# Kernel tuning notes

Hardware: AMD Instinct MI355X
Metric: run time of the kernel (lower is better)

The kernel has to match this reference:

```python
import jax, jax.numpy as jnp
import numpy as np

ND, NP_, ED, EP, B = 8192, 8192, 262144, 262144, 4096
DIM = 300 + 1024 + 1024 + 1024  # 3372
EPS = 1e-5


def _bn(x, g, b):
    # BatchNorm1d in training mode: biased batch statistics
    m = x.mean(0)
    v = x.var(0)
    return (x - m) * jax.lax.rsqrt(v + EPS) * g + b


def _gcn(x, ei, ew, W, bias):
    # PyG GCNConv: add self-loops (weight 1), symmetric deg^-1/2 normalization,
    # linear transform, scatter-add aggregation at target nodes.
    N = x.shape[0]
    loop = jnp.arange(N)
    src = jnp.concatenate([ei[0], loop])
    dst = jnp.concatenate([ei[1], loop])
    w = jnp.concatenate([ew, jnp.ones((N,), ew.dtype)])
    deg = jax.ops.segment_sum(w, dst, num_segments=N)
    dinv = jnp.where(deg > 0, jax.lax.rsqrt(deg), 0.0)
    norm = dinv[src] * w * dinv[dst]          # [E+N]
    h = x @ W                                  # [N, 512]
    out = jax.ops.segment_sum(h[src] * norm[:, None], dst, num_segments=N) + bias
    return jax.nn.leaky_relu(out, 0.01)


def setup_inputs() -> dict:
    key = jax.random.key(0)
    ks = jax.random.split(key, 32)
    s = 0.02
    inp = {
        'd_index': jax.random.randint(ks[0], (B,), 0, ND),
        'p_index': jax.random.randint(ks[1], (B,), 0, NP_),
        'd_vecs': jax.random.normal(ks[2], (B, 300), jnp.float32),
        'p_embeddings': jax.random.normal(ks[3], (B, 1024), jnp.float32),
        'd_ecfps': jax.random.uniform(ks[4], (ND, 1024), jnp.float32),
        'd_ei': jax.random.randint(ks[5], (2, ED), 0, ND),
        'd_ew': jax.random.uniform(ks[6], (ED,), jnp.float32),
        'p_gos': jax.random.uniform(ks[7], (NP_, 1024), jnp.float32),
        'p_ei': jax.random.randint(ks[8], (2, EP), 0, NP_),
        'p_ew': jax.random.uniform(ks[9], (EP,), jnp.float32),
        'affinity': jax.random.uniform(ks[10], (ND, NP_), jnp.float32),
        # GCNConv params
        'W_e': jax.random.normal(ks[11], (1024, 512), jnp.float32) * s,
        'b_e': jnp.zeros((512,), jnp.float32),
        'W_g': jax.random.normal(ks[12], (1024, 512), jnp.float32) * s,
        'b_g': jnp.zeros((512,), jnp.float32),
        # lin1 / lin2
        'W1': jax.random.normal(ks[13], (512, 512), jnp.float32) * s,
        'b1': jnp.zeros((512,), jnp.float32),
        'W2': jax.random.normal(ks[14], (512, 512), jnp.float32) * s,
        'b2': jnp.zeros((512,), jnp.float32),
        # output MLP: 3372 -> 1024 -> 256 -> 1 with BN+ReLU (dropout = eval identity)
        'Wo1': jax.random.normal(ks[15], (DIM, 1024), jnp.float32) * s,
        'bo1': jnp.zeros((1024,), jnp.float32),
        'g1': jnp.ones((1024,), jnp.float32),
        'be1': jnp.zeros((1024,), jnp.float32),
        'Wo2': jax.random.normal(ks[16], (1024, 256), jnp.float32) * s,
        'bo2': jnp.zeros((256,), jnp.float32),
        'g2': jnp.ones((256,), jnp.float32),
        'be2': jnp.zeros((256,), jnp.float32),
        'Wo3': jax.random.normal(ks[17], (256, 1), jnp.float32) * s,
        'bo3': jnp.zeros((1,), jnp.float32),
    }
    return inp


def reference(d_index, p_index, d_vecs, p_embeddings, d_ecfps, d_ei, d_ew,
              p_gos, p_ei, p_ew, affinity,
              W_e, b_e, W_g, b_g, W1, b1, W2, b2,
              Wo1, bo1, g1, be1, Wo2, bo2, g2, be2, Wo3, bo3):
    ecfps = _gcn(d_ecfps, d_ei, d_ew, W_e, b_e)          # [ND, 512]
    gos = _gcn(p_gos, p_ei, p_ew, W_g, b_g)              # [NP, 512]
    drug = ecfps[d_index]                                 # [B, 512]
    protein = gos[p_index]                                # [B, 512]
    p2d = jax.nn.relu((affinity @ gos) @ W1 + b1)[d_index]      # [B, 512]
    d2p = jax.nn.relu((affinity.T @ ecfps) @ W2 + b2)[p_index]  # [B, 512]
    drug = jnp.concatenate([drug, p2d], axis=1)
    protein = jnp.concatenate([protein, d2p], axis=1)
    feature = jnp.concatenate([d_vecs, p_embeddings, drug, protein], axis=1)  # [B, 3372]
    h = jax.nn.relu(_bn(feature @ Wo1 + bo1, g1, be1))
    h = jax.nn.relu(_bn(h @ Wo2 + bo2, g2, be2))
    y = h @ Wo3 + bo3                                     # [B, 1]
    return y
```

## Files before the change

kernel.cpp:

```cpp
#include <hip/hip_runtime.h>
#include <stdint.h>
#include <stddef.h>

typedef unsigned short u16;
typedef unsigned int u32;
typedef __attribute__((ext_vector_type(8))) short bf16x8;
typedef __attribute__((ext_vector_type(8))) u16 u16x8;
typedef __attribute__((ext_vector_type(4))) float f32x4;

#define NDN 8192
#define NPN 8192
#define EDN 262144
#define EPN 262144
#define BBN 4096
#define KPAD 3392

__device__ __forceinline__ u16 f2b(float f) {
  u32 u = __float_as_uint(f);
  u32 r = (u + 0x7fffu + ((u >> 16) & 1u)) >> 16;
  return (u16)r;
}
__device__ __forceinline__ float b2f(u16 h) {
  return __uint_as_float(((u32)h) << 16);
}

__device__ __forceinline__ void gld_lds16(const void* g, void* l) {
  __builtin_amdgcn_global_load_lds(
      (const __attribute__((address_space(1))) u32*)g,
      (__attribute__((address_space(3))) u32*)l, 16, 0, 0);
}

template<int BM, int BN, int WM, int WN>
__global__ void __launch_bounds__(256, 2)
gemm_bf16(const u16* __restrict__ A, int lda,
          const u16* __restrict__ Bt, int ldb,
          int N, int K,
          float* __restrict__ Cf, u16* __restrict__ Cb,
          const float* __restrict__ bias,
          const float* __restrict__ rowscale,
          int relu)
{
  constexpr int AISS = BM / 32;
  constexpr int BISS = BN / 32;
  constexpr int AF = WM / 16;
  constexpr int BF = WN / 16;
  constexpr int WGN = BN / WN;
  __shared__ __align__(16) u16 ldsA[BM * 64];
  __shared__ __align__(16) u16 ldsB[BN * 64];
  const int t = threadIdx.x;
  const int lane = t & 63;
  const int w = t >> 6;
  const int m0 = blockIdx.x * BM;
  const int n0 = blockIdx.y * BN;
  const int wm = w / WGN, wn = w % WGN;
  const int sr = t >> 3;
  const int sk = (t & 7) * 8;

  const u16* arow[AISS];
#pragma unroll
  for (int j = 0; j < AISS; ++j)
    arow[j] = A + (long)(m0 + j * 32 + sr) * lda + sk;
  const u16* brow[BISS];
#pragma unroll
  for (int j = 0; j < BISS; ++j)
    brow[j] = Bt + (long)(n0 + j * 32 + sr) * ldb + sk;

  f32x4 acc[AF][BF];
#pragma unroll
  for (int i = 0; i < AF; ++i)
#pragma unroll
    for (int j = 0; j < BF; ++j)
      acc[i][j] = (f32x4){0.f, 0.f, 0.f, 0.f};

  for (int k0 = 0; k0 < K; k0 += 64) {
#pragma unroll
    for (int j = 0; j < AISS; ++j)
      gld_lds16(arow[j] + k0, &ldsA[(j * 32 + w * 8) * 64]);
#pragma unroll
    for (int j = 0; j < BISS; ++j)
      gld_lds16(brow[j] + k0, &ldsB[(j * 32 + w * 8) * 64]);
    __syncthreads();
#pragma unroll
    for (int k2 = 0; k2 < 64; k2 += 32) {
      bf16x8 af[AF], bfv[BF];
#pragma unroll
      for (int i = 0; i < AF; ++i)
        af[i] = *(const bf16x8*)&ldsA[(wm * WM + i * 16 + (lane & 15)) * 64 + k2 + (lane >> 4) * 8];
#pragma unroll
      for (int i = 0; i < BF; ++i)
        bfv[i] = *(const bf16x8*)&ldsB[(wn * WN + i * 16 + (lane & 15)) * 64 + k2 + (lane >> 4) * 8];
#pragma unroll
      for (int i = 0; i < AF; ++i)
#pragma unroll
        for (int j = 0; j < BF; ++j)
          acc[i][j] = __builtin_amdgcn_mfma_f32_16x16x32_bf16(af[i], bfv[j], acc[i][j], 0, 0, 0);
    }
    __syncthreads();
  }

  const int er = (lane >> 4) * 4;
  const int ecn = lane & 15;
#pragma unroll
  for (int i = 0; i < AF; ++i)
#pragma unroll
    for (int j = 0; j < BF; ++j)
#pragma unroll
      for (int r = 0; r < 4; ++r) {
        long gm = m0 + wm * WM + i * 16 + er + r;
        long gn = n0 + wn * WN + j * 16 + ecn;
        float v = acc[i][j][r];
        if (bias) v += bias[gn];
        if (rowscale) v *= rowscale[gm];
        if (relu) v = fmaxf(v, 0.f);
        if (Cb) Cb[gm * N + gn] = f2b(v);
        else    Cf[gm * N + gn] = v;
      }
}

template<bool TRANSA>
__global__ void __launch_bounds__(256, 2)
gemm_a32(const float* __restrict__ A, int lda,
         const u16* __restrict__ Bt, int ldb,
         int N, int K,
         const int* __restrict__ idx,
         float* __restrict__ Cf, long zstride)
{
  constexpr int AF = 2, BF = 8, WGN = 2;
  __shared__ __align__(16) u16 ldsA[64 * 72];
  __shared__ __align__(16) u16 ldsB[256 * 64];
  __shared__ __align__(16) float ldsF[TRANSA ? 64 * 64 : 16];
  const int t = threadIdx.x;
  const int lane = t & 63;
  const int w = t >> 6;
  const int m0 = blockIdx.x * 64;
  const int n0 = blockIdx.y * 256;
  const int kOff = blockIdx.z * K;
  const int wm = w / WGN, wn = w % WGN;
  const int sr = t >> 3;
  const int sk = (t & 7) * 8;

  Cf += (long)blockIdx.z * zstride;

  const u16* brow[8];
#pragma unroll
  for (int j = 0; j < 8; ++j)
    brow[j] = Bt + (long)(n0 + j * 32 + sr) * ldb + sk + kOff;

  long rowsel = 0;
  if (!TRANSA) {
    int r = m0 + (t >> 2);
    rowsel = idx ? (long)idx[r] : (long)r;
  }
  const float* ar_direct = A + rowsel * (long)lda + (t & 3) * 16 + kOff;

  f32x4 acc[AF][BF];
#pragma unroll
  for (int i = 0; i < AF; ++i)
#pragma unroll
    for (int j = 0; j < BF; ++j)
      acc[i][j] = (f32x4){0.f, 0.f, 0.f, 0.f};

  for (int k0 = 0; k0 < K; k0 += 64) {
#pragma unroll
    for (int j = 0; j < 8; ++j)
      gld_lds16(brow[j] + k0, &ldsB[(j * 32 + w * 8) * 64]);

    if (TRANSA) {
#pragma unroll
      for (int j = 0; j < 4; ++j) {
        int cc = w * 4 + j;
        int d = cc * 4 + (lane >> 4);
        gld_lds16(A + (long)(kOff + k0 + d) * lda + m0 + (lane & 15) * 4,
                  &ldsF[cc * 256]);
      }
      __syncthreads();
      {
        int pp = t & 63, c0 = (t >> 6) * 16;
        float vv[16];
#pragma unroll
        for (int i = 0; i < 16; ++i) vv[i] = ldsF[(c0 + i) * 64 + pp];
        u16x8 ua, ub;
#pragma unroll
        for (int i = 0; i < 8; ++i) { ua[i] = f2b(vv[i]); ub[i] = f2b(vv[8 + i]); }
        *(u16x8*)&ldsA[pp * 72 + c0] = ua;
        *(u16x8*)&ldsA[pp * 72 + c0 + 8] = ub;
      }
    } else {
      const float4* src = (const float4*)(ar_direct + k0);
      float4 v0 = src[0], v1 = src[1], v2 = src[2], v3 = src[3];
      u16x8 ua, ub;
      ua[0] = f2b(v0.x); ua[1] = f2b(v0.y); ua[2] = f2b(v0.z); ua[3] = f2b(v0.w);
      ua[4] = f2b(v1.x); ua[5] = f2b(v1.y); ua[6] = f2b(v1.z); ua[7] = f2b(v1.w);
      ub[0] = f2b(v2.x); ub[1] = f2b(v2.y); ub[2] = f2b(v2.z); ub[3] = f2b(v2.w);
      ub[4] = f2b(v3.x); ub[5] = f2b(v3.y); ub[6] = f2b(v3.w == v3.w ? v3.w : v3.w);
      ub[6] = f2b(v3.z); ub[7] = f2b(v3.w);
      ub[0] = f2b(v2.x); ub[1] = f2b(v2.y); ub[2] = f2b(v2.z); ub[3] = f2b(v2.w);
      ub[4] = f2b(v3.x); ub[5] = f2b(v3.y); ub[6] = f2b(v3.z); ub[7] = f2b(v3.w);
      int ro = (t >> 2) * 72 + (t & 3) * 16;
      *(u16x8*)&ldsA[ro] = ua;
      *(u16x8*)&ldsA[ro + 8] = ub;
      __syncthreads();
    }
    if (TRANSA) __syncthreads();
    else __syncthreads();
#pragma unroll
    for (int k2 = 0; k2 < 64; k2 += 32) {
      bf16x8 af[AF], bfv[BF];
#pragma unroll
      for (int i = 0; i < AF; ++i)
        af[i] = *(const bf16x8*)&ldsA[(wm * 32 + i * 16 + (lane & 15)) * 72 + k2 + (lane >> 4) * 8];
#pragma unroll
      for (int i = 0; i < BF; ++i)
        bfv[i] = *(const bf16x8*)&ldsB[(wn * 128 + i * 16 + (lane & 15)) * 64 + k2 + (lane >> 4) * 8];
#pragma unroll
      for (int i = 0; i < AF; ++i)
#pragma unroll
        for (int j = 0; j < BF; ++j)
          acc[i][j] = __builtin_amdgcn_mfma_f32_16x16x32_bf16(af[i], bfv[j], acc[i][j], 0, 0, 0);
    }
    __syncthreads();
  }

  const int er = (lane >> 4) * 4;
  const int ecn = lane & 15;
#pragma unroll
  for (int i = 0; i < AF; ++i)
#pragma unroll
    for (int j = 0; j < BF; ++j)
#pragma unroll
      for (int r = 0; r < 4; ++r) {
        long gm = m0 + wm * 32 + i * 16 + er + r;
        long gn = n0 + wn * 128 + j * 16 + ecn;
        Cf[gm * N + gn] = acc[i][j][r];
      }
}

__global__ void reduceP(const float* __restrict__ p, long n, int parts,
                        float* __restrict__ out) {
  long i = ((long)blockIdx.x * 256 + threadIdx.x) * 4;
  if (i >= n) return;
  float4 a = *(const float4*)&p[i];
  for (int z = 1; z < parts; ++z) {
    float4 b = *(const float4*)&p[(long)z * n + i];
    a.x += b.x; a.y += b.y; a.z += b.z; a.w += b.w;
  }
  *(float4*)&out[i] = a;
}

__global__ void __launch_bounds__(256, 2)
gemm_sp(const float* __restrict__ A, int lda,
        const u16* __restrict__ Bt, int ldb,
        int N, int K,
        const int* __restrict__ idx,
        const float* __restrict__ bias,
        float* __restrict__ Cf)
{
  __shared__ __align__(16) u16 ldsAh[64 * 64];
  __shared__ __align__(16) u16 ldsAl[64 * 64];
  __shared__ __align__(16) u16 ldsB[64 * 64];
  const int t = threadIdx.x, lane = t & 63, w = t >> 6;
  const int m0 = blockIdx.x * 64, n0 = blockIdx.y * 64;
  const int wm = w >> 1, wn = w & 1;
  const int sr = t >> 3, sk = (t & 7) * 8;
  const int ar = t >> 2;
  const int ak = (t & 3) * 16;
  long arow = idx ? (long)idx[m0 + ar] : (long)(m0 + ar);
  const float* Ap = A + arow * (long)lda + ak;
  const u16* brow[2];
#pragma unroll
  for (int j = 0; j < 2; ++j)
    brow[j] = Bt + (long)(n0 + j * 32 + sr) * ldb + sk;

  f32x4 acc[2][2];
#pragma unroll
  for (int i = 0; i < 2; ++i)
#pragma unroll
    for (int j = 0; j < 2; ++j)
      acc[i][j] = (f32x4){0.f, 0.f, 0.f, 0.f};

  for (int k0 = 0; k0 < K; k0 += 64) {
#pragma unroll
    for (int j = 0; j < 2; ++j)
      gld_lds16(brow[j] + k0, &ldsB[(j * 32 + w * 8) * 64]);
    const float4* src = (const float4*)(Ap + k0);
    float4 v0 = src[0], v1 = src[1], v2 = src[2], v3 = src[3];
    float f[16] = {v0.x, v0.y, v0.z, v0.w, v1.x, v1.y, v1.z, v1.w,
                   v2.x, v2.y, v2.z, v2.w, v3.x, v3.y, v3.z, v3.w};
    u16x8 h0, h1v, l0, l1v;
#pragma unroll
    for (int i = 0; i < 8; ++i) {
      u16 h = f2b(f[i]);       h0[i] = h;  l0[i] = f2b(f[i] - b2f(h));
      u16 g = f2b(f[8 + i]);   h1v[i] = g; l1v[i] = f2b(f[8 + i] - b2f(g));
    }
    *(u16x8*)&ldsAh[ar * 64 + ak] = h0;
    *(u16x8*)&ldsAh[ar * 64 + ak + 8] = h1v;
    *(u16x8*)&ldsAl[ar * 64 + ak] = l0;
    *(u16x8*)&ldsAl[ar * 64 + ak + 8] = l1v;
    __syncthreads();
#pragma unroll
    for (int k2 = 0; k2 < 64; k2 += 32) {
      bf16x8 ah[2], al[2], bv[2];
#pragma unroll
      for (int i = 0; i < 2; ++i) {
        int off = (wm * 32 + i * 16 + (lane & 15)) * 64 + k2 + (lane >> 4) * 8;
        ah[i] = *(const bf16x8*)&ldsAh[off];
        al[i] = *(const bf16x8*)&ldsAl[off];
      }
#pragma unroll
      for (int i = 0; i < 2; ++i)
        bv[i] = *(const bf16x8*)&ldsB[(wn * 32 + i * 16 + (lane & 15)) * 64 + k2 + (lane >> 4) * 8];
#pragma unroll
      for (int i = 0; i < 2; ++i)
#pragma unroll
        for (int j = 0; j < 2; ++j) {
          acc[i][j] = __builtin_amdgcn_mfma_f32_16x16x32_bf16(ah[i], bv[j], acc[i][j], 0, 0, 0);
          acc[i][j] = __builtin_amdgcn_mfma_f32_16x16x32_bf16(al[i], bv[j], acc[i][j], 0, 0, 0);
        }
    }
    __syncthreads();
  }

  const int er = (lane >> 4) * 4;
  const int ecn = lane & 15;
#pragma unroll
  for (int i = 0; i < 2; ++i)
#pragma unroll
    for (int j = 0; j < 2; ++j)
#pragma unroll
      for (int r = 0; r < 4; ++r) {
        long gm = m0 + wm * 32 + i * 16 + er + r;
        long gn = n0 + wn * 32 + j * 16 + ecn;
        float v = acc[i][j][r] + bias[gn];
        Cf[gm * N + gn] = fmaxf(v, 0.f);
      }
}

__global__ void cvt_bf16(const float* __restrict__ x, u16* __restrict__ y, long n) {
  long i = ((long)blockIdx.x * 256 + threadIdx.x) * 4;
  if (i < n) {
    float4 v = *(const float4*)&x[i];
    u16 a = f2b(v.x), b = f2b(v.y), c = f2b(v.z), d = f2b(v.w);
    u32 lo = (u32)a | ((u32)b << 16);
    u32 hi = (u32)c | ((u32)d << 16);
    *(uint2*)&y[i] = make_uint2(lo, hi);
  }
}

__global__ void wtrans(const float* __restrict__ in, u16* __restrict__ out,
                       int R, int C, int Rpad) {
  __shared__ float tile[32][33];
  int r0 = blockIdx.x * 32, c0 = blockIdx.y * 32;
  int tx = threadIdx.x & 31, ty = threadIdx.x >> 5;
  for (int j = 0; j < 32; j += 8) {
    int r = r0 + ty + j, c = c0 + tx;
    tile[ty + j][tx] = (r < R && c < C) ? in[(long)r * C + c] : 0.f;
  }
  __syncthreads();
  for (int j = 0; j < 32; j += 8) {
    int c = c0 + ty + j, r = r0 + tx;
    if (c < C && r < Rpad) out[(long)c * Rpad + r] = f2b(tile[tx][ty + j]);
  }
}

__global__ void btrans(const u16* __restrict__ in, u16* __restrict__ out, int R, int C) {
  __shared__ u16 tile[32][34];
  int r0 = blockIdx.x * 32, c0 = blockIdx.y * 32;
  int tx = threadIdx.x & 31, ty = threadIdx.x >> 5;
  for (int j = 0; j < 32; j += 8)
    tile[ty + j][tx] = in[(long)(r0 + ty + j) * C + c0 + tx];
  __syncthreads();
  for (int j = 0; j < 32; j += 8)
    out[(long)(c0 + ty + j) * R + r0 + tx] = tile[tx][ty + j];
}

__global__ void edge_deg(const int* __restrict__ ei, const float* __restrict__ ew,
                         int E, float* degw, int* cnt) {
  int e = blockIdx.x * 256 + threadIdx.x;
  if (e < E) {
    int dst = ei[E + e];
    atomicAdd(&degw[dst], ew[e]);
    atomicAdd(&cnt[dst], 1);
  }
}

__global__ void make_dinv(const float* __restrict__ degw, float* __restrict__ dinv, int N) {
  int i = blockIdx.x * 256 + threadIdx.x;
  if (i < N) dinv[i] = rsqrtf(degw[i] + 1.0f);
}

__global__ void scan8k(const int* __restrict__ cnt, int* __restrict__ rowptr,
                       int* __restrict__ cursor) {
  __shared__ int lds[256];
  int t = threadIdx.x;
  int c0 = t * 32;
  int loc[32];
  int s = 0;
#pragma unroll
  for (int i = 0; i < 32; ++i) { loc[i] = cnt[c0 + i]; s += loc[i]; }
  lds[t] = s;
  __syncthreads();
  for (int off = 1; off < 256; off <<= 1) {
    int add = (t >= off) ? lds[t - off] : 0;
    __syncthreads();
    lds[t] += add;
    __syncthreads();
  }
  int run = lds[t] - s;
#pragma unroll
  for (int i = 0; i < 32; ++i) {
    rowptr[c0 + i] = run;
    cursor[c0 + i] = run;
    run += loc[i];
  }
  if (t == 255) rowptr[8192] = run;
}

__global__ void edge_scatter(const int* __restrict__ ei, const float* __restrict__ ew,
                             int E, int* __restrict__ cursor, int2* __restrict__ edges) {
  int e = blockIdx.x * 256 + threadIdx.x;
  if (e < E) {
    int src = ei[e], dst = ei[E + e];
    int pos = atomicAdd(&cursor[dst], 1);
    edges[pos] = make_int2(src, __float_as_int(ew[e]));
  }
}

__global__ void gcn_aggregate(const u16* __restrict__ hs,
                              const int* __restrict__ rowptr,
                              const int2* __restrict__ edges,
                              const float* __restrict__ dinv,
                              const float* __restrict__ bias,
                              u16* __restrict__ out) {
  const int i = blockIdx.x;
  const int t = threadIdx.x;
  const u32* base = (const u32*)hs;
  u32 hv = base[i * 256 + t];
  float a0 = b2f((u16)(hv & 0xffff));
  float a1 = b2f((u16)(hv >> 16));
  int s = rowptr[i], e = rowptr[i + 1];
  int p = s;
  for (; p + 4 <= e; p += 4) {
    int2 e0 = edges[p], e1 = edges[p + 1], e2 = edges[p + 2], e3 = edges[p + 3];
    u32 v0 = base[(long)e0.x * 256 + t];
    u32 v1 = base[(long)e1.x * 256 + t];
    u32 v2 = base[(long)e2.x * 256 + t];
    u32 v3 = base[(long)e3.x * 256 + t];
    float w0 = __int_as_float(e0.y), w1 = __int_as_float(e1.y);
    float w2 = __int_as_float(e2.y), w3 = __int_as_float(e3.y);
    a0 += w0 * b2f((u16)(v0 & 0xffff)); a1 += w0 * b2f((u16)(v0 >> 16));
    a0 += w1 * b2f((u16)(v1 & 0xffff)); a1 += w1 * b2f((u16)(v1 >> 16));
    a0 += w2 * b2f((u16)(v2 & 0xffff)); a1 += w2 * b2f((u16)(v2 >> 16));
    a0 += w3 * b2f((u16)(v3 & 0xffff)); a1 += w3 * b2f((u16)(v3 >> 16));
  }
  for (; p < e; ++p) {
    int2 ee = edges[p];
    u32 v = base[(long)ee.x * 256 + t];
    float ww = __int_as_float(ee.y);
    a0 += ww * b2f((u16)(v & 0xffff));
    a1 += ww * b2f((u16)(v >> 16));
  }
  float di = dinv[i];
  float o0 = bias[2 * t] + di * a0;
  float o1 = bias[2 * t + 1] + di * a1;
  o0 = (o0 >= 0.f) ? o0 : 0.01f * o0;
  o1 = (o1 >= 0.f) ? o1 : 0.01f * o1;
  ((u32*)out)[i * 256 + t] = (u32)f2b(o0) | ((u32)f2b(o1) << 16);
}

__global__ void colsum_f32(const float* __restrict__ src, int ld, int cols,
                           const int* __restrict__ idx, float* __restrict__ out) {
  int c = blockIdx.x * 256 + threadIdx.x;
  if (c >= cols) return;
  int r0 = blockIdx.y * 128;
  float s = 0.f;
  for (int r = r0; r < r0 + 128; ++r) {
    long row = idx ? (long)idx[r] : (long)r;
    s += src[row * ld + c];
  }
  atomicAdd(&out[c], s);
}

__global__ void colsum_b16(const u16* __restrict__ src, int ld, int cols,
                           const int* __restrict__ idx, float* __restrict__ out) {
  int c = blockIdx.x * 256 + threadIdx.x;
  if (c >= cols) return;
  int r0 = blockIdx.y * 128;
  float s = 0.f;
  for (int r = r0; r < r0 + 128; ++r) {
    long row = idx ? (long)idx[r] : (long)r;
    s += b2f(src[row * ld + c]);
  }
  atomicAdd(&out[c], s);
}

__global__ void assemble(const float* __restrict__ d_vecs, const float* __restrict__ p_emb,
                         const u16* __restrict__ ec, const u16* __restrict__ gos,
                         const float* __restrict__ t1, const float* __restrict__ t2,
                         const int* __restrict__ didx, const int* __restrict__ pidx,
                         const float* __restrict__ cs, u16* __restrict__ feat) {
  const float is = 1.f / 4096.f;
  int b = blockIdx.x;
  int t = threadIdx.x;
  long ob = (long)b * KPAD;
  int di = didx[b], pi = pidx[b];
  for (int j = t; j < 300; j += 256)
    feat[ob + j] = f2b(d_vecs[(long)b * 300 + j] - cs[j] * is);
  for (int j = t; j < 1024; j += 256)
    feat[ob + 300 + j] = f2b(p_emb[(long)b * 1024 + j] - cs[300 + j] * is);
  for (int j = t; j < 512; j += 256) {
    feat[ob + 1324 + j] = f2b(b2f(ec[(long)di * 512 + j]) - cs[1324 + j] * is);
    feat[ob + 1836 + j] = f2b(t1[(long)b * 512 + j] - cs[1836 + j] * is);
    feat[ob + 2348 + j] = f2b(b2f(gos[(long)pi * 512 + j]) - cs[2348 + j] * is);
    feat[ob + 2860 + j] = f2b(t2[(long)b * 512 + j] - cs[2860 + j] * is);
  }
  for (int j = t; j < 20; j += 256) feat[ob + 3372 + j] = 0;
}

__global__ void bn_stats(const float* __restrict__ x, int N,
                         float* __restrict__ sum, float* __restrict__ sumsq) {
  int r0 = blockIdx.x * 64;
  int t = threadIdx.x;
  for (int c = t; c < N; c += 256) {
    float s = 0.f, q = 0.f;
    for (int r = 0; r < 64; ++r) {
      float v = x[(long)(r0 + r) * N + c];
      s += v; q += v * v;
    }
    atomicAdd(&sum[c], s);
    atomicAdd(&sumsq[c], q);
  }
}

__global__ void bn_apply(const float* __restrict__ x, int M, int N, int nmask,
                         const float* __restrict__ sum, const float* __restrict__ sumsq,
                         const float* __restrict__ g, const float* __restrict__ be,
                         u16* __restrict__ y) {
  long i = (long)blockIdx.x * 256 + threadIdx.x;
  if (i >= (long)M * N) return;
  int c = (int)(i & nmask);
  float m = sum[c] / (float)M;
  float v = sumsq[c] / (float)M - m * m;
  float sc = g[c] * rsqrtf(v + 1e-5f);
  float sh = be[c] - m * sc;
  float o = fmaxf(x[i] * sc + sh, 0.f);
  y[i] = f2b(o);
}

__global__ void final_dot(const u16* __restrict__ h, const float* __restrict__ w,
                          const float* __restrict__ b0, float* __restrict__ y) {
  int wv = threadIdx.x >> 6, lane = threadIdx.x & 63;
  int row = blockIdx.x * 4 + wv;
  const u16* hr = h + (long)row * 256;
  ushort4 u = *(const ushort4*)&hr[lane * 4];
  float acc = b2f(u.x) * w[lane * 4] + b2f(u.y) * w[lane * 4 + 1] +
              b2f(u.z) * w[lane * 4 + 2] + b2f(u.w) * w[lane * 4 + 3];
  for (int off = 32; off; off >>= 1) acc += __shfl_down(acc, off);
  if (lane == 0) y[row] = acc + b0[0];
}

extern "C" void kernel_launch(void* const* d_in, const int* in_sizes, int n_in,
                              void* d_out, int out_size, void* d_ws, size_t ws_size,
                              hipStream_t stream) {
  (void)in_sizes; (void)n_in; (void)out_size; (void)ws_size;
  const int*   d_index  = (const int*)d_in[0];
  const int*   p_index  = (const int*)d_in[1];
  const float* d_vecs   = (const float*)d_in[2];
  const float* p_emb    = (const float*)d_in[3];
  const float* d_ecfps  = (const float*)d_in[4];
  const int*   d_ei     = (const int*)d_in[5];
  const float* d_ew     = (const float*)d_in[6];
  const float* p_gos    = (const float*)d_in[7];
  const int*   p_ei     = (const int*)d_in[8];
  const float* p_ew     = (const float*)d_in[9];
  const float* affinity = (const float*)d_in[10];
  const float* W_e  = (const float*)d_in[11];
  const float* b_e  = (const float*)d_in[12];
  const float* W_g  = (const float*)d_in[13];
  const float* b_g  = (const float*)d_in[14];
  const float* W1   = (const float*)d_in[15];
  const float* b1   = (const float*)d_in[16];
  const float* W2   = (const float*)d_in[17];
  const float* b2   = (const float*)d_in[18];
  const float* Wo1  = (const float*)d_in[19];
  const float* bo1  = (const float*)d_in[20];
  const float* g1   = (const float*)d_in[21];
  const float* be1  = (const float*)d_in[22];
  const float* Wo2  = (const float*)d_in[23];
  const float* bo2  = (const float*)d_in[24];
  const float* g2   = (const float*)d_in[25];
  const float* be2  = (const float*)d_in[26];
  const float* Wo3  = (const float*)d_in[27];
  const float* bo3  = (const float*)d_in[28];
  float* y_out = (float*)d_out;

  char* p = (char*)d_ws;
  auto alloc = [&](size_t bytes) -> char* {
    char* q = p;
    p += (bytes + 255) & ~(size_t)255;
    return q;
  };

  char* zero_start = p;
  float* degw_e = (float*)alloc(NDN * 4);
  int*   cnt_e  = (int*)alloc(NDN * 4);
  float* degw_p = (float*)alloc(NPN * 4);
  int*   cnt_p  = (int*)alloc(NPN * 4);
  float* bnsum1 = (float*)alloc(1024 * 4);
  float* bnsq1  = (float*)alloc(1024 * 4);
  float* bnsum2 = (float*)alloc(256 * 4);
  float* bnsq2  = (float*)alloc(256 * 4);
  float* colsum = (float*)alloc(KPAD * 4);
  size_t zero_bytes = (size_t)(p - zero_start);

  float* dinv_e   = (float*)alloc(NDN * 4);
  float* dinv_p   = (float*)alloc(NPN * 4);
  int*   rowptr_e = (int*)alloc((NDN + 1) * 4);
  int*   cursor_e = (int*)alloc(NDN * 4);
  int*   rowptr_p = (int*)alloc((NPN + 1) * 4);
  int*   cursor_p = (int*)alloc(NPN * 4);
  int2*  edges_e  = (int2*)alloc((size_t)EDN * 8);
  int2*  edges_p  = (int2*)alloc((size_t)EPN * 8);
  u16* x_e_b  = (u16*)alloc((size_t)NDN * 1024 * 2);
  u16* x_g_b  = (u16*)alloc((size_t)NPN * 1024 * 2);
  u16* WeT    = (u16*)alloc((size_t)512 * 1024 * 2);
  u16* WgT    = (u16*)alloc((size_t)512 * 1024 * 2);
  u16* W1T    = (u16*)alloc((size_t)512 * 512 * 2);
  u16* W2T    = (u16*)alloc((size_t)512 * 512 * 2);
  u16* Wo1T   = (u16*)alloc((size_t)1024 * KPAD * 2);
  u16* Wo2T   = (u16*)alloc((size_t)256 * 1024 * 2);
  u16* hs_e   = (u16*)alloc((size_t)NDN * 512 * 2);
  u16* hs_g   = (u16*)alloc((size_t)NPN * 512 * 2);
  u16* ec_b   = (u16*)alloc((size_t)NDN * 512 * 2);
  u16* gos_b  = (u16*)alloc((size_t)NPN * 512 * 2);
  u16* ecT_b  = (u16*)alloc((size_t)512 * NDN * 2);
  u16* gosT_b = (u16*)alloc((size_t)512 * NPN * 2);
  u16* feat_b = (u16*)alloc((size_t)BBN * KPAD * 2);
  float* h1   = (float*)alloc((size_t)BBN * 1024 * 4);
  u16* h1n_b  = (u16*)alloc((size_t)BBN * 1024 * 2);
  float* h2   = (float*)alloc((size_t)BBN * 256 * 4);
  u16* h2n_b  = (u16*)alloc((size_t)BBN * 256 * 2);
  float* partK = (float*)alloc((size_t)4 * BBN * 512 * 4);

  float* tmp1_f = (float*)x_e_b;
  float* tmp2_f = (float*)x_g_b;
  float* t1_f   = (float*)hs_e;
  float* t2_f   = (float*)hs_g;

  hipMemsetAsync(zero_start, 0, zero_bytes, stream);

  cvt_bf16<<<8192, 256, 0, stream>>>(d_ecfps, x_e_b, (long)NDN * 1024);
  cvt_bf16<<<8192, 256, 0, stream>>>(p_gos, x_g_b, (long)NPN * 1024);
  wtrans<<<dim3(32, 16), 256, 0, stream>>>(W_e, WeT, 1024, 512, 1024);
  wtrans<<<dim3(32, 16), 256, 0, stream>>>(W_g, WgT, 1024, 512, 1024);
  wtrans<<<dim3(16, 16), 256, 0, stream>>>(W1, W1T, 512, 512, 512);
  wtrans<<<dim3(16, 16), 256, 0, stream>>>(W2, W2T, 512, 512, 512);
  wtrans<<<dim3(106, 32), 256, 0, stream>>>(Wo1, Wo1T, 3372, 1024, KPAD);
  wtrans<<<dim3(32, 8), 256, 0, stream>>>(Wo2, Wo2T, 1024, 256, 1024);

  edge_deg<<<EDN / 256, 256, 0, stream>>>(d_ei, d_ew, EDN, degw_e, cnt_e);
  edge_deg<<<EPN / 256, 256, 0, stream>>>(p_ei, p_ew, EPN, degw_p, cnt_p);
  make_dinv<<<NDN / 256, 256, 0, stream>>>(degw_e, dinv_e, NDN);
  make_dinv<<<NPN / 256, 256, 0, stream>>>(degw_p, dinv_p, NPN);
  scan8k<<<1, 256, 0, stream>>>(cnt_e, rowptr_e, cursor_e);
  scan8k<<<1, 256, 0, stream>>>(cnt_p, rowptr_p, cursor_p);
  edge_scatter<<<EDN / 256, 256, 0, stream>>>(d_ei, d_ew, EDN, cursor_e, edges_e);
  edge_scatter<<<EPN / 256, 256, 0, stream>>>(p_ei, p_ew, EPN, cursor_p, edges_p);

  gemm_bf16<64, 128, 32, 64><<<dim3(128, 4), 256, 0, stream>>>(
      x_e_b, 1024, WeT, 1024, 512, 1024,
      (float*)nullptr, hs_e, (const float*)nullptr, dinv_e, 0);
  gemm_bf16<64, 128, 32, 64><<<dim3(128, 4), 256, 0, stream>>>(
      x_g_b, 1024, WgT, 1024, 512, 1024,
      (float*)nullptr, hs_g, (const float*)nullptr, dinv_p, 0);

  gcn_aggregate<<<NDN, 256, 0, stream>>>(hs_e, rowptr_e, edges_e, dinv_e, b_e, ec_b);
  gcn_aggregate<<<NPN, 256, 0, stream>>>(hs_g, rowptr_p, edges_p, dinv_p, b_g, gos_b);

  btrans<<<dim3(256, 16), 256, 0, stream>>>(ec_b, ecT_b, NDN, 512);
  btrans<<<dim3(256, 16), 256, 0, stream>>>(gos_b, gosT_b, NPN, 512);

  gemm_a32<false><<<dim3(64, 2, 4), 256, 0, stream>>>(
      affinity, 8192, gosT_b, 8192, 512, 2048, d_index, partK, (long)BBN * 512);
  reduceP<<<2048, 256, 0, stream>>>(partK, (long)BBN * 512, 4, tmp1_f);

  gemm_a32<true><<<dim3(128, 2, 2), 256, 0, stream>>>(
      affinity, 8192, ecT_b, 8192, 512, 4096, (const int*)nullptr,
      partK, (long)NDN * 512);
  reduceP<<<4096, 256, 0, stream>>>(partK, (long)NDN * 512, 2, tmp2_f);

  gemm_sp<<<dim3(64, 8), 256, 0, stream>>>(
      tmp1_f, 512, W1T, 512, 512, 512, (const int*)nullptr, b1, t1_f);
  gemm_sp<<<dim3(64, 8), 256, 0, stream>>>(
      tmp2_f, 512, W2T, 512, 512, 512, p_index, b2, t2_f);

  colsum_f32<<<dim3(2, 32),  256, 0, stream>>>(d_vecs, 300, 300, nullptr, colsum);
  colsum_f32<<<dim3(4, 32),  256, 0, stream>>>(p_emb, 1024, 1024, nullptr, colsum + 300);
  colsum_b16<<<dim3(2, 32),  256, 0, stream>>>(ec_b, 512, 512, d_index, colsum + 1324);
  colsum_f32<<<dim3(2, 32),  256, 0, stream>>>(t1_f, 512, 512, nullptr, colsum + 1836);
  colsum_b16<<<dim3(2, 32),  256, 0, stream>>>(gos_b, 512, 512, p_index, colsum + 2348);
  colsum_f32<<<dim3(2, 32),  256, 0, stream>>>(t2_f, 512, 512, nullptr, colsum + 2860);

  assemble<<<BBN, 256, 0, stream>>>(d_vecs, p_emb, ec_b, gos_b, t1_f, t2_f,
                                    d_index, p_index, colsum, feat_b);

  gemm_bf16<64, 128, 32, 64><<<dim3(64, 8), 256, 0, stream>>>(
      feat_b, KPAD, Wo1T, KPAD, 1024, KPAD,
      h1, (u16*)nullptr, bo1, (const float*)nullptr, 0);
  bn_stats<<<64, 256, 0, stream>>>(h1, 1024, bnsum1, bnsq1);
  bn_apply<<<16384, 256, 0, stream>>>(h1, BBN, 1024, 1023, bnsum1, bnsq1, g1, be1, h1n_b);

  gemm_bf16<64, 64, 32, 32><<<dim3(64, 4), 256, 0, stream>>>(
      h1n_b, 1024, Wo2T, 1024, 256, 1024,
      h2, (u16*)nullptr, bo2, (const float*)nullptr, 0);
  bn_stats<<<64, 256, 0, stream>>>(h2, 256, bnsum2, bnsq2);
  bn_apply<<<4096, 256, 0, stream>>>(h2, BBN, 256, 255, bnsum2, bnsq2, g2, be2, h2n_b);

  final_dot<<<1024, 256, 0, stream>>>(h2n_b, Wo3, bo3, y_out);
}
```

Measured before the change: 1.177 ms.

## Gather d2p rows before GEMM, split-K Wo1, fuse graph prep and colsum kernels

The affinity^T @ ecfps product now covers only the B gathered protein rows. Affinity is first transposed and converted to a bf16 copy, then a gathered bf16 GEMM runs over 4096 rows instead of all 8192. The Wo1 GEMM is split along K with a reduction that adds the bias. The edge-degree, scan/dinv, edge-scatter and six colsum kernels are each merged into single launches, and the occupancy hint and bn_stats grid are raised. The cost is a full 8192x8192 transpose-convert pass and a 128MB buffer, which may offset the halved GEMM work.

```diff
diff --git a/kernel.cpp b/kernel.cpp
--- a/kernel.cpp
+++ b/kernel.cpp
@@ -30,12 +30,13 @@
       (__attribute__((address_space(3))) u32*)l, 16, 0, 0);
 }
 
-template<int BM, int BN, int WM, int WN>
-__global__ void __launch_bounds__(256, 2)
+template<int BM, int BN, int WM, int WN, bool GATHER>
+__global__ void __launch_bounds__(256, 3)
 gemm_bf16(const u16* __restrict__ A, int lda,
           const u16* __restrict__ Bt, int ldb,
-          int N, int K,
-          float* __restrict__ Cf, u16* __restrict__ Cb,
+          int N, int K, int KZ,
+          const int* __restrict__ idx,
+          float* __restrict__ Cf, u16* __restrict__ Cb, long zstride,
           const float* __restrict__ bias,
           const float* __restrict__ rowscale,
           int relu)
@@ -52,18 +53,25 @@
   const int w = t >> 6;
   const int m0 = blockIdx.x * BM;
   const int n0 = blockIdx.y * BN;
+  const int kOff = blockIdx.z * KZ;
+  const int Kloc = min(KZ, K - kOff);
   const int wm = w / WGN, wn = w % WGN;
   const int sr = t >> 3;
   const int sk = (t & 7) * 8;
 
+  if (zstride) Cf += (long)blockIdx.z * zstride;
+
   const u16* arow[AISS];
 #pragma unroll
-  for (int j = 0; j < AISS; ++j)
-    arow[j] = A + (long)(m0 + j * 32 + sr) * lda + sk;
+  for (int j = 0; j < AISS; ++j) {
+    int r = m0 + j * 32 + sr;
+    long rr = GATHER ? (long)idx[r] : (long)r;
+    arow[j] = A + rr * (long)lda + sk + kOff;
+  }
   const u16* brow[BISS];
 #pragma unroll
   for (int j = 0; j < BISS; ++j)
-    brow[j] = Bt + (long)(n0 + j * 32 + sr) * ldb + sk;
+    brow[j] = Bt + (long)(n0 + j * 32 + sr) * ldb + sk + kOff;
 
   f32x4 acc[AF][BF];
 #pragma unroll
@@ -72,7 +80,7 @@
     for (int j = 0; j < BF; ++j)
       acc[i][j] = (f32x4){0.f, 0.f, 0.f, 0.f};
 
-  for (int k0 = 0; k0 < K; k0 += 64) {
+  for (int k0 = 0; k0 < Kloc; k0 += 64) {
 #pragma unroll
     for (int j = 0; j < AISS; ++j)
       gld_lds16(arow[j] + k0, &ldsA[(j * 32 + w * 8) * 64]);
@@ -117,24 +125,22 @@
       }
 }
 
-template<bool TRANSA>
-__global__ void __launch_bounds__(256, 2)
-gemm_a32(const float* __restrict__ A, int lda,
-         const u16* __restrict__ Bt, int ldb,
-         int N, int K,
-         const int* __restrict__ idx,
-         float* __restrict__ Cf, long zstride)
+__global__ void __launch_bounds__(256, 3)
+gemm_a32g(const float* __restrict__ A, int lda,
+          const u16* __restrict__ Bt, int ldb,
+          int N, int KZ,
+          const int* __restrict__ idx,
+          float* __restrict__ Cf, long zstride)
 {
   constexpr int AF = 2, BF = 8, WGN = 2;
   __shared__ __align__(16) u16 ldsA[64 * 72];
   __shared__ __align__(16) u16 ldsB[256 * 64];
-  __shared__ __align__(16) float ldsF[TRANSA ? 64 * 64 : 16];
   const int t = threadIdx.x;
   const int lane = t & 63;
   const int w = t >> 6;
   const int m0 = blockIdx.x * 64;
   const int n0 = blockIdx.y * 256;
-  const int kOff = blockIdx.z * K;
+  const int kOff = blockIdx.z * KZ;
   const int wm = w / WGN, wn = w % WGN;
   const int sr = t >> 3;
   const int sk = (t & 7) * 8;
@@ -146,11 +152,8 @@
   for (int j = 0; j < 8; ++j)
     brow[j] = Bt + (long)(n0 + j * 32 + sr) * ldb + sk + kOff;
 
-  long rowsel = 0;
-  if (!TRANSA) {
-    int r = m0 + (t >> 2);
-    rowsel = idx ? (long)idx[r] : (long)r;
-  }
+  int r = m0 + (t >> 2);
+  long rowsel = idx ? (long)idx[r] : (long)r;
   const float* ar_direct = A + rowsel * (long)lda + (t & 3) * 16 + kOff;
 
   f32x4 acc[AF][BF];
@@ -160,49 +163,22 @@
     for (int j = 0; j < BF; ++j)
       acc[i][j] = (f32x4){0.f, 0.f, 0.f, 0.f};
 
-  for (int k0 = 0; k0 < K; k0 += 64) {
+  for (int k0 = 0; k0 < KZ; k0 += 64) {
 #pragma unroll
     for (int j = 0; j < 8; ++j)
       gld_lds16(brow[j] + k0, &ldsB[(j * 32 + w * 8) * 64]);
 
-    if (TRANSA) {
-#pragma unroll
-      for (int j = 0; j < 4; ++j) {
-        int cc = w * 4 + j;
-        int d = cc * 4 + (lane >> 4);
-        gld_lds16(A + (long)(kOff + k0 + d) * lda + m0 + (lane & 15) * 4,
-                  &ldsF[cc * 256]);
-      }
-      __syncthreads();
-      {
-        int pp = t & 63, c0 = (t >> 6) * 16;
-        float vv[16];
-#pragma unroll
-        for (int i = 0; i < 16; ++i) vv[i] = ldsF[(c0 + i) * 64 + pp];
-        u16x8 ua, ub;
-#pragma unroll
-        for (int i = 0; i < 8; ++i) { ua[i] = f2b(vv[i]); ub[i] = f2b(vv[8 + i]); }
-        *(u16x8*)&ldsA[pp * 72 + c0] = ua;
-        *(u16x8*)&ldsA[pp * 72 + c0 + 8] = ub;
-      }
-    } else {
-      const float4* src = (const float4*)(ar_direct + k0);
-      float4 v0 = src[0], v1 = src[1], v2 = src[2], v3 = src[3];
-      u16x8 ua, ub;
-      ua[0] = f2b(v0.x); ua[1] = f2b(v0.y); ua[2] = f2b(v0.z); ua[3] = f2b(v0.w);
-      ua[4] = f2b(v1.x); ua[5] = f2b(v1.y); ua[6] = f2b(v1.z); ua[7] = f2b(v1.w);
-      ub[0] = f2b(v2.x); ub[1] = f2b(v2.y); ub[2] = f2b(v2.z); ub[3] = f2b(v2.w);
-      ub[4] = f2b(v3.x); ub[5] = f2b(v3.y); ub[6] = f2b(v3.w == v3.w ? v3.w : v3.w);
-      ub[6] = f2b(v3.z); ub[7] = f2b(v3.w);
-      ub[0] = f2b(v2.x); ub[1] = f2b(v2.y); ub[2] = f2b(v2.z); ub[3] = f2b(v2.w);
-      ub[4] = f2b(v3.x); ub[5] = f2b(v3.y); ub[6] = f2b(v3.z); ub[7] = f2b(v3.w);
-      int ro = (t >> 2) * 72 + (t & 3) * 16;
-      *(u16x8*)&ldsA[ro] = ua;
-      *(u16x8*)&ldsA[ro + 8] = ub;
-      __syncthreads();
-    }
-    if (TRANSA) __syncthreads();
-    else __syncthreads();
+    const float4* src = (const float4*)(ar_direct + k0);
+    float4 v0 = src[0], v1 = src[1], v2 = src[2], v3 = src[3];
+    u16x8 ua, ub;
+    ua[0] = f2b(v0.x); ua[1] = f2b(v0.y); ua[2] = f2b(v0.z); ua[3] = f2b(v0.w);
+    ua[4] = f2b(v1.x); ua[5] = f2b(v1.y); ua[6] = f2b(v1.z); ua[7] = f2b(v1.w);
+    ub[0] = f2b(v2.x); ub[1] = f2b(v2.y); ub[2] = f2b(v2.z); ub[3] = f2b(v2.w);
+    ub[4] = f2b(v3.x); ub[5] = f2b(v3.y); ub[6] = f2b(v3.z); ub[7] = f2b(v3.w);
+    int ro = (t >> 2) * 72 + (t & 3) * 16;
+    *(u16x8*)&ldsA[ro] = ua;
+    *(u16x8*)&ldsA[ro + 8] = ub;
+    __syncthreads();
 #pragma unroll
     for (int k2 = 0; k2 < 64; k2 += 32) {
       bf16x8 af[AF], bfv[BF];
@@ -228,14 +204,15 @@
 #pragma unroll
     for (int j = 0; j < BF; ++j)
 #pragma unroll
-      for (int r = 0; r < 4; ++r) {
-        long gm = m0 + wm * 32 + i * 16 + er + r;
+      for (int rr2 = 0; rr2 < 4; ++rr2) {
+        long gm = m0 + wm * 32 + i * 16 + er + rr2;
         long gn = n0 + wn * 128 + j * 16 + ecn;
-        Cf[gm * N + gn] = acc[i][j][r];
+        Cf[gm * N + gn] = acc[i][j][rr2];
       }
 }
 
 __global__ void reduceP(const float* __restrict__ p, long n, int parts,
+                        int nmask, const float* __restrict__ bias,
                         float* __restrict__ out) {
   long i = ((long)blockIdx.x * 256 + threadIdx.x) * 4;
   if (i >= n) return;
@@ -244,14 +221,45 @@
     float4 b = *(const float4*)&p[(long)z * n + i];
     a.x += b.x; a.y += b.y; a.z += b.z; a.w += b.w;
   }
+  if (bias) {
+    int c = (int)(i & nmask);
+    a.x += bias[c]; a.y += bias[c + 1]; a.z += bias[c + 2]; a.w += bias[c + 3];
+  }
   *(float4*)&out[i] = a;
+}
+
+__global__ void __launch_bounds__(256)
+transcvt(const float* __restrict__ in, u16* __restrict__ out) {
+  __shared__ float tile[64][65];
+  const int t = threadIdx.x;
+  const int r0 = blockIdx.x * 64, c0 = blockIdx.y * 64;
+  {
+    int rr = t >> 2, cb = (t & 3) * 16;
+    const float4* src = (const float4*)&in[(long)(r0 + rr) * 8192 + c0 + cb];
+    float4 a = src[0], b = src[1], c = src[2], d = src[3];
+    float* dst = &tile[rr][cb];
+    *(float4*)(dst) = a; *(float4*)(dst + 4) = b;
+    *(float4*)(dst + 8) = c; *(float4*)(dst + 12) = d;
+  }
+  __syncthreads();
+  {
+    int cc = t >> 2, rb = (t & 3) * 16;
+    u16x8 ua, ub;
+#pragma unroll
+    for (int j = 0; j < 8; ++j) {
+      ua[j] = f2b(tile[rb + j][cc]);
+      ub[j] = f2b(tile[rb + 8 + j][cc]);
+    }
+    u16* dst = &out[(long)(c0 + cc) * 8192 + r0 + rb];
+    *(u16x8*)dst = ua;
+    *(u16x8*)(dst + 8) = ub;
+  }
 }
 
 __global__ void __launch_bounds__(256, 2)
 gemm_sp(const float* __restrict__ A, int lda,
         const u16* __restrict__ Bt, int ldb,
         int N, int K,
-        const int* __restrict__ idx,
         const float* __restrict__ bias,
         float* __restrict__ Cf)
 {
@@ -264,8 +272,7 @@
   const int sr = t >> 3, sk = (t & 7) * 8;
   const int ar = t >> 2;
   const int ak = (t & 3) * 16;
-  long arow = idx ? (long)idx[m0 + ar] : (long)(m0 + ar);
-  const float* Ap = A + arow * (long)lda + ak;
+  const float* Ap = A + (long)(m0 + ar) * lda + ak;
   const u16* brow[2];
 #pragma unroll
   for (int j = 0; j < 2; ++j)
@@ -373,23 +380,30 @@
     out[(long)(c0 + ty + j) * R + r0 + tx] = tile[tx][ty + j];
 }
 
-__global__ void edge_deg(const int* __restrict__ ei, const float* __restrict__ ew,
-                         int E, float* degw, int* cnt) {
+__global__ void edge_deg2(const int* __restrict__ ei_a, const float* __restrict__ ew_a,
+                          const int* __restrict__ ei_b, const float* __restrict__ ew_b,
+                          int E, float* degw_a, int* cnt_a,
+                          float* degw_b, int* cnt_b) {
   int e = blockIdx.x * 256 + threadIdx.x;
-  if (e < E) {
-    int dst = ei[E + e];
-    atomicAdd(&degw[dst], ew[e]);
-    atomicAdd(&cnt[dst], 1);
-  }
-}
-
-__global__ void make_dinv(const float* __restrict__ degw, float* __restrict__ dinv, int N) {
-  int i = blockIdx.x * 256 + threadIdx.x;
-  if (i < N) dinv[i] = rsqrtf(degw[i] + 1.0f);
-}
-
-__global__ void scan8k(const int* __restrict__ cnt, int* __restrict__ rowptr,
-                       int* __restrict__ cursor) {
+  if (e >= E) return;
+  const int* ei = blockIdx.y ? ei_b : ei_a;
+  const float* ew = blockIdx.y ? ew_b : ew_a;
+  float* degw = blockIdx.y ? degw_b : degw_a;
+  int* cnt = blockIdx.y ? cnt_b : cnt_a;
+  int dst = ei[E + e];
+  atomicAdd(&degw[dst], ew[e]);
+  atomicAdd(&cnt[dst], 1);
+}
+
+__global__ void scan_dinv(const int* __restrict__ cnt_a, int* rowptr_a, int* cursor_a,
+                          const float* __restrict__ degw_a, float* dinv_a,
+                          const int* __restrict__ cnt_b, int* rowptr_b, int* cursor_b,
+                          const float* __restrict__ degw_b, float* dinv_b) {
+  const int* cnt = blockIdx.x ? cnt_b : cnt_a;
+  int* rowptr = blockIdx.x ? rowptr_b : rowptr_a;
+  int* cursor = blockIdx.x ? cursor_b : cursor_a;
+  const float* degw = blockIdx.x ? degw_b : degw_a;
+  float* dinv = blockIdx.x ? dinv_b : dinv_a;
   __shared__ int lds[256];
   int t = threadIdx.x;
   int c0 = t * 32;
@@ -413,16 +427,24 @@
     run += loc[i];
   }
   if (t == 255) rowptr[8192] = run;
-}
-
-__global__ void edge_scatter(const int* __restrict__ ei, const float* __restrict__ ew,
-                             int E, int* __restrict__ cursor, int2* __restrict__ edges) {
+#pragma unroll
+  for (int i = 0; i < 32; ++i)
+    dinv[c0 + i] = rsqrtf(degw[c0 + i] + 1.0f);
+}
+
+__global__ void edge_scatter2(const int* __restrict__ ei_a, const float* __restrict__ ew_a,
+                              const int* __restrict__ ei_b, const float* __restrict__ ew_b,
+                              int E, int* cursor_a, int2* edges_a,
+                              int* cursor_b, int2* edges_b) {
   int e = blockIdx.x * 256 + threadIdx.x;
-  if (e < E) {
-    int src = ei[e], dst = ei[E + e];
-    int pos = atomicAdd(&cursor[dst], 1);
-    edges[pos] = make_int2(src, __float_as_int(ew[e]));
-  }
+  if (e >= E) return;
+  const int* ei = blockIdx.y ? ei_b : ei_a;
+  const float* ew = blockIdx.y ? ew_b : ew_a;
+  int* cursor = blockIdx.y ? cursor_b : cursor_a;
+  int2* edges = blockIdx.y ? edges_b : edges_a;
+  int src = ei[e], dst = ei[E + e];
+  int pos = atomicAdd(&cursor[dst], 1);
+  edges[pos] = make_int2(src, __float_as_int(ew[e]));
 }
 
 __global__ void gcn_aggregate(const u16* __restrict__ hs,
@@ -467,28 +489,32 @@
   ((u32*)out)[i * 256 + t] = (u32)f2b(o0) | ((u32)f2b(o1) << 16);
 }
 
-__global__ void colsum_f32(const float* __restrict__ src, int ld, int cols,
-                           const int* __restrict__ idx, float* __restrict__ out) {
+__global__ void colsum_all(const float* __restrict__ d_vecs, const float* __restrict__ p_emb,
+                           const u16* __restrict__ ec, const u16* __restrict__ gos,
+                           const float* __restrict__ t1, const float* __restrict__ t2,
+                           const int* __restrict__ didx, const int* __restrict__ pidx,
+                           float* __restrict__ out) {
   int c = blockIdx.x * 256 + threadIdx.x;
-  if (c >= cols) return;
+  if (c >= 3372) return;
   int r0 = blockIdx.y * 128;
   float s = 0.f;
-  for (int r = r0; r < r0 + 128; ++r) {
-    long row = idx ? (long)idx[r] : (long)r;
-    s += src[row * ld + c];
-  }
-  atomicAdd(&out[c], s);
-}
-
-__global__ void colsum_b16(const u16* __restrict__ src, int ld, int cols,
-                           const int* __restrict__ idx, float* __restrict__ out) {
-  int c = blockIdx.x * 256 + threadIdx.x;
-  if (c >= cols) return;
-  int r0 = blockIdx.y * 128;
-  float s = 0.f;
-  for (int r = r0; r < r0 + 128; ++r) {
-    long row = idx ? (long)idx[r] : (long)r;
-    s += b2f(src[row * ld + c]);
+  if (c < 300) {
+    for (int r = r0; r < r0 + 128; ++r) s += d_vecs[(long)r * 300 + c];
+  } else if (c < 1324) {
+    int cc = c - 300;
+    for (int r = r0; r < r0 + 128; ++r) s += p_emb[(long)r * 1024 + cc];
+  } else if (c < 1836) {
+    int cc = c - 1324;
+    for (int r = r0; r < r0 + 128; ++r) s += b2f(ec[(long)didx[r] * 512 + cc]);
+  } else if (c < 2348) {
+    int cc = c - 1836;
+    for (int r = r0; r < r0 + 128; ++r) s += t1[(long)r * 512 + cc];
+  } else if (c < 2860) {
+    int cc = c - 2348;
+    for (int r = r0; r < r0 + 128; ++r) s += b2f(gos[(long)pidx[r] * 512 + cc]);
+  } else {
+    int cc = c - 2860;
+    for (int r = r0; r < r0 + 128; ++r) s += t2[(long)r * 512 + cc];
   }
   atomicAdd(&out[c], s);
 }
@@ -518,11 +544,11 @@
 
 __global__ void bn_stats(const float* __restrict__ x, int N,
                          float* __restrict__ sum, float* __restrict__ sumsq) {
-  int r0 = blockIdx.x * 64;
+  int r0 = blockIdx.x * 32;
   int t = threadIdx.x;
   for (int c = t; c < N; c += 256) {
     float s = 0.f, q = 0.f;
-    for (int r = 0; r < 64; ++r) {
+    for (int r = 0; r < 32; ++r) {
       float v = x[(long)(r0 + r) * N + c];
       s += v; q += v * v;
     }
@@ -634,6 +660,7 @@
   u16* gos_b  = (u16*)alloc((size_t)NPN * 512 * 2);
   u16* ecT_b  = (u16*)alloc((size_t)512 * NDN * 2);
   u16* gosT_b = (u16*)alloc((size_t)512 * NPN * 2);
+  u16* affT_b = (u16*)alloc((size_t)8192 * 8192 * 2);
   u16* feat_b = (u16*)alloc((size_t)BBN * KPAD * 2);
   float* h1   = (float*)alloc((size_t)BBN * 1024 * 4);
   u16* h1n_b  = (u16*)alloc((size_t)BBN * 1024 * 2);
@@ -657,21 +684,22 @@
   wtrans<<<dim3(106, 32), 256, 0, stream>>>(Wo1, Wo1T, 3372, 1024, KPAD);
   wtrans<<<dim3(32, 8), 256, 0, stream>>>(Wo2, Wo2T, 1024, 256, 1024);
 
-  edge_deg<<<EDN / 256, 256, 0, stream>>>(d_ei, d_ew, EDN, degw_e, cnt_e);
-  edge_deg<<<EPN / 256, 256, 0, stream>>>(p_ei, p_ew, EPN, degw_p, cnt_p);
-  make_dinv<<<NDN / 256, 256, 0, stream>>>(degw_e, dinv_e, NDN);
-  make_dinv<<<NPN / 256, 256, 0, stream>>>(degw_p, dinv_p, NPN);
-  scan8k<<<1, 256, 0, stream>>>(cnt_e, rowptr_e, cursor_e);
-  scan8k<<<1, 256, 0, stream>>>(cnt_p, rowptr_p, cursor_p);
-  edge_scatter<<<EDN / 256, 256, 0, stream>>>(d_ei, d_ew, EDN, cursor_e, edges_e);
-  edge_scatter<<<EPN / 256, 256, 0, stream>>>(p_ei, p_ew, EPN, cursor_p, edges_p);
-
-  gemm_bf16<64, 128, 32, 64><<<dim3(128, 4), 256, 0, stream>>>(
-      x_e_b, 1024, WeT, 1024, 512, 1024,
-      (float*)nullptr, hs_e, (const float*)nullptr, dinv_e, 0);
-  gemm_bf16<64, 128, 32, 64><<<dim3(128, 4), 256, 0, stream>>>(
-      x_g_b, 1024, WgT, 1024, 512, 1024,
-      (float*)nullptr, hs_g, (const float*)nullptr, dinv_p, 0);
+  transcvt<<<dim3(128, 128), 256, 0, stream>>>(affinity, affT_b);
+
+  edge_deg2<<<dim3(EDN / 256, 2), 256, 0, stream>>>(d_ei, d_ew, p_ei, p_ew, EDN,
+                                                    degw_e, cnt_e, degw_p, cnt_p);
+  scan_dinv<<<2, 256, 0, stream>>>(cnt_e, rowptr_e, cursor_e, degw_e, dinv_e,
+                                   cnt_p, rowptr_p, cursor_p, degw_p, dinv_p);
+  edge_scatter2<<<dim3(EDN / 256, 2), 256, 0, stream>>>(d_ei, d_ew, p_ei, p_ew, EDN,
+                                                        cursor_e, edges_e,
+                                                        cursor_p, edges_p);
+
+  gemm_bf16<64, 128, 32, 64, false><<<dim3(128, 4), 256, 0, stream>>>(
+      x_e_b, 1024, WeT, 1024, 512, 1024, 1024, nullptr,
+      (float*)nullptr, hs_e, 0, (const float*)nullptr, dinv_e, 0);
+  gemm_bf16<64, 128, 32, 64, false><<<dim3(128, 4), 256, 0, stream>>>(
+      x_g_b, 1024, WgT, 1024, 512, 1024, 1024, nullptr,
+      (float*)nullptr, hs_g, 0, (const float*)nullptr, dinv_p, 0);
 
   gcn_aggregate<<<NDN, 256, 0, stream>>>(hs_e, rowptr_e, edges_e, dinv_e, b_e, ec_b);
   gcn_aggregate<<<NPN, 256, 0, stream>>>(hs_g, rowptr_p, edges_p, dinv_p, b_g, gos_b);
@@ -679,40 +707,39 @@
   btrans<<<dim3(256, 16), 256, 0, stream>>>(ec_b, ecT_b, NDN, 512);
   btrans<<<dim3(256, 16), 256, 0, stream>>>(gos_b, gosT_b, NPN, 512);
 
-  gemm_a32<false><<<dim3(64, 2, 4), 256, 0, stream>>>(
+  gemm_a32g<<<dim3(64, 2, 4), 256, 0, stream>>>(
       affinity, 8192, gosT_b, 8192, 512, 2048, d_index, partK, (long)BBN * 512);
-  reduceP<<<2048, 256, 0, stream>>>(partK, (long)BBN * 512, 4, tmp1_f);
-
-  gemm_a32<true><<<dim3(128, 2, 2), 256, 0, stream>>>(
-      affinity, 8192, ecT_b, 8192, 512, 4096, (const int*)nullptr,
-      partK, (long)NDN * 512);
-  reduceP<<<4096, 256, 0, stream>>>(partK, (long)NDN * 512, 2, tmp2_f);
+  reduceP<<<2048, 256, 0, stream>>>(partK, (long)BBN * 512, 4, 0, nullptr, tmp1_f);
+
+  gemm_bf16<64, 128, 32, 64, true><<<dim3(64, 4, 2), 256, 0, stream>>>(
+      affT_b, 8192, ecT_b, 8192, 512, 8192, 4096, p_index,
+      partK, (u16*)nullptr, (long)BBN * 512,
+      (const float*)nullptr, (const float*)nullptr, 0);
+  reduceP<<<2048, 256, 0, stream>>>(partK, (long)BBN * 512, 2, 0, nullptr, tmp2_f);
 
   gemm_sp<<<dim3(64, 8), 256, 0, stream>>>(
-      tmp1_f, 512, W1T, 512, 512, 512, (const int*)nullptr, b1, t1_f);
+      tmp1_f, 512, W1T, 512, 512, 512, b1, t1_f);
   gemm_sp<<<dim3(64, 8), 256, 0, stream>>>(
-      tmp2_f, 512, W2T, 512, 512, 512, p_index, b2, t2_f);
-
-  colsum_f32<<<dim3(2, 32),  256, 0, stream>>>(d_vecs, 300, 300, nullptr, colsum);
-  colsum_f32<<<dim3(4, 32),  256, 0, stream>>>(p_emb, 1024, 1024, nullptr, colsum + 300);
-  colsum_b16<<<dim3(2, 32),  256, 0, stream>>>(ec_b, 512, 512, d_index, colsum + 1324);
-  colsum_f32<<<dim3(2, 32),  256, 0, stream>>>(t1_f, 512, 512, nullptr, colsum + 1836);
-  colsum_b16<<<dim3(2, 32),  256, 0, stream>>>(gos_b, 512, 512, p_index, colsum + 2348);
-  colsum_f32<<<dim3(2, 32),  256, 0, stream>>>(t2_f, 512, 512, nullptr, colsum + 2860);
+      tmp2_f, 512, W2T, 512, 512, 512, b2, t2_f);
+
+  colsum_all<<<dim3(14, 32), 256, 0, stream>>>(d_vecs, p_emb, ec_b, gos_b,
+                                               t1_f, t2_f, d_index, p_index, colsum);
 
   assemble<<<BBN, 256, 0, stream>>>(d_vecs, p_emb, ec_b, gos_b, t1_f, t2_f,
                                     d_index, p_index, colsum, feat_b);
 
-  gemm_bf16<64, 128, 32, 64><<<dim3(64, 8), 256, 0, stream>>>(
-      feat_b, KPAD, Wo1T, KPAD, 1024, KPAD,
-      h1, (u16*)nullptr, bo1, (const float*)nullptr, 0);
-  bn_stats<<<64, 256, 0, stream>>>(h1, 1024, bnsum1, bnsq1);
+  gemm_bf16<64, 128, 32, 64, false><<<dim3(64, 8, 2), 256, 0, stream>>>(
+      feat_b, KPAD, Wo1T, KPAD, 1024, KPAD, 1728, nullptr,
+      partK, (u16*)nullptr, (long)BBN * 1024,
+      (const float*)nullptr, (const float*)nullptr, 0);
+  reduceP<<<4096, 256, 0, stream>>>(partK, (long)BBN * 1024, 2, 1023, bo1, h1);
+  bn_stats<<<128, 256, 0, stream>>>(h1, 1024, bnsum1, bnsq1);
   bn_apply<<<16384, 256, 0, stream>>>(h1, BBN, 1024, 1023, bnsum1, bnsq1, g1, be1, h1n_b);
 
-  gemm_bf16<64, 64, 32, 32><<<dim3(64, 4), 256, 0, stream>>>(
-      h1n_b, 1024, Wo2T, 1024, 256, 1024,
-      h2, (u16*)nullptr, bo2, (const float*)nullptr, 0);
-  bn_stats<<<64, 256, 0, stream>>>(h2, 256, bnsum2, bnsq2);
+  gemm_bf16<64, 64, 32, 32, false><<<dim3(64, 4), 256, 0, stream>>>(
+      h1n_b, 1024, Wo2T, 1024, 256, 1024, 1024, nullptr,
+      h2, (u16*)nullptr, 0, bo2, (const float*)nullptr, 0);
+  bn_stats<<<128, 256, 0, stream>>>(h2, 256, bnsum2, bnsq2);
   bn_apply<<<4096, 256, 0, stream>>>(h2, BBN, 256, 255, bnsum2, bnsq2, g2, be2, h2n_b);
 
   final_dot<<<1024, 256, 0, stream>>>(h2n_b, Wo3, bo3, y_out);
```

Measured after the change: 1.123 ms. -4.6%, faster.
